# Kernel tuning notes

Hardware: AMD Instinct MI355X
Metric: run time of the kernel (lower is better)

The kernel has to match this reference:

```python
import jax, jax.numpy as jnp
import numpy as np

B = 4096
IN_DIMS = (3, 32, 32)      # in_numel = 3072
OUT_DIMS = (64, 16, 16)    # out_numel = 16384
IN_NUMEL = int(np.prod(IN_DIMS))
OUT_NUMEL = int(np.prod(OUT_DIMS))


def setup_inputs() -> dict:
    key = jax.random.key(0)
    k1, k2, k3, k4 = jax.random.split(key, 4)
    x = jax.random.normal(k1, (B,) + IN_DIMS, dtype=jnp.float32)
    # Cached composed linear operator (out_numel x in_numel); scale ~1/sqrt(fan_in)
    cached_matrix = jax.random.normal(k2, (OUT_NUMEL, IN_NUMEL), dtype=jnp.float32) / np.sqrt(IN_NUMEL)
    cached_matrix_extra = jax.random.uniform(k3, (1,), dtype=jnp.float32) + 0.5
    cached_tensor_extra = jax.random.normal(k4, (IN_NUMEL, IN_NUMEL), dtype=jnp.float32) / IN_NUMEL
    return {
        "x": x,
        "cached_matrix": cached_matrix,
        "cached_matrix_extra": cached_matrix_extra,
        "cached_tensor_extra": cached_tensor_extra,
    }


def reference(x, cached_matrix, cached_matrix_extra, cached_tensor_extra):
    batches = x.shape[0]
    # input_as_matrix: [in_numel, B]
    X = x.reshape(batches, -1).T
    # input_as_matrix_extra: L2 norm per column -> [1, B]
    X_extra = jnp.linalg.norm(X, ord=2, axis=0, keepdims=True)
    # output_as_matrix = M @ X : [out_numel, B]
    Y = jnp.matmul(cached_matrix, X)
    # output_as_matrix_extra = s * ||x|| + sum((T @ X) * X, axis=0)
    Y_extra = cached_matrix_extra * X_extra + jnp.sum(jnp.matmul(cached_tensor_extra, X) * X, axis=0, keepdims=True)
    Y = Y / Y_extra
    return Y.T.reshape(batches, *OUT_DIMS)
```

## Files before the change

kernel.cpp:

```cpp
#include <hip/hip_runtime.h>
#include <hip/hip_bf16.h>

typedef __attribute__((ext_vector_type(8))) short bf16x8;
typedef __attribute__((ext_vector_type(4))) short bf16x4;
typedef __attribute__((ext_vector_type(4))) float f32x4;

#define DEV __device__ __forceinline__

static constexpr int BATCH = 4096;
static constexpr int KDIM  = 3072;
static constexpr int NOUT  = 16384;

DEV unsigned short f2bf(float f) {
  union { float f; unsigned int u; } v; v.f = f;
  unsigned int u = v.u;
  u += 0x7fffu + ((u >> 16) & 1u);
  return (unsigned short)(u >> 16);
}

__global__ __launch_bounds__(256) void prep_x_kernel(
    const float* __restrict__ x, unsigned short* __restrict__ xbf,
    float* __restrict__ nrm) {
  const int b = blockIdx.x;
  const int t = threadIdx.x;
  const float* row = x + (size_t)b * KDIM;
  unsigned short* orow = xbf + (size_t)b * KDIM;
  float ss = 0.f;
#pragma unroll
  for (int i = 0; i < 3; ++i) {
    const int c = i * 256 + t;
    float4 v = reinterpret_cast<const float4*>(row)[c];
    ss += v.x * v.x + v.y * v.y + v.z * v.z + v.w * v.w;
    bf16x4 o;
    o[0] = (short)f2bf(v.x); o[1] = (short)f2bf(v.y);
    o[2] = (short)f2bf(v.z); o[3] = (short)f2bf(v.w);
    reinterpret_cast<bf16x4*>(orow)[c] = o;
  }
#pragma unroll
  for (int off = 32; off > 0; off >>= 1) ss += __shfl_down(ss, off, 64);
  __shared__ float red[4];
  if ((t & 63) == 0) red[t >> 6] = ss;
  __syncthreads();
  if (t == 0) nrm[b] = sqrtf(red[0] + red[1] + red[2] + red[3]);
}

__global__ __launch_bounds__(256) void cvt_kernel(
    const float* __restrict__ src, unsigned short* __restrict__ dst, size_t n4) {
  size_t i = (size_t)blockIdx.x * blockDim.x + threadIdx.x;
  const size_t stride = (size_t)gridDim.x * blockDim.x;
  for (; i < n4; i += stride) {
    float4 v = reinterpret_cast<const float4*>(src)[i];
    bf16x4 o;
    o[0] = (short)f2bf(v.x); o[1] = (short)f2bf(v.y);
    o[2] = (short)f2bf(v.z); o[3] = (short)f2bf(v.w);
    reinterpret_cast<bf16x4*>(dst)[i] = o;
  }
}

__global__ __launch_bounds__(256) void qform_kernel(
    const unsigned short* __restrict__ A,
    const unsigned short* __restrict__ Bm,
    const float* __restrict__ xf,
    float* __restrict__ partial) {
  __shared__ unsigned short ldsA[128 * 32];
  __shared__ unsigned short ldsB[128 * 32];
  const int t = threadIdx.x;
  const int lane = t & 63;
  const int wv = t >> 6;
  const int wr = wv >> 1, wc = wv & 1;
  const int col0 = blockIdx.x * 128;
  const int row0 = blockIdx.y * 128;

  f32x4 acc[4][4];
#pragma unroll
  for (int i = 0; i < 4; ++i)
#pragma unroll
    for (int j = 0; j < 4; ++j) acc[i][j] = (f32x4){0.f, 0.f, 0.f, 0.f};

  const unsigned short* aBase = A + (size_t)row0 * KDIM;
  const unsigned short* bBase = Bm + (size_t)col0 * KDIM;
  const int ldsoff0 = (t & ~63) * 8;

  for (int k0 = 0; k0 < KDIM; k0 += 32) {
    __syncthreads();
#pragma unroll
    for (int i = 0; i < 2; ++i) {
      const int c = i * 256 + t;
      const unsigned short* ga = aBase + (size_t)(c >> 2) * KDIM + (k0 + (c & 3) * 8);
      const unsigned short* gb = bBase + (size_t)(c >> 2) * KDIM + (k0 + (c & 3) * 8);
      __builtin_amdgcn_global_load_lds(
          (const __attribute__((address_space(1))) unsigned int*)(const void*)ga,
          (__attribute__((address_space(3))) unsigned int*)(void*)(ldsA + i * 2048 + ldsoff0),
          16, 0, 0);
      __builtin_amdgcn_global_load_lds(
          (const __attribute__((address_space(1))) unsigned int*)(const void*)gb,
          (__attribute__((address_space(3))) unsigned int*)(void*)(ldsB + i * 2048 + ldsoff0),
          16, 0, 0);
    }
    __syncthreads();
    bf16x8 af[4], bfr[4];
#pragma unroll
    for (int mi = 0; mi < 4; ++mi)
      af[mi] = *reinterpret_cast<const bf16x8*>(
          &ldsA[(wr * 64 + mi * 16 + (lane & 15)) * 32 + (lane >> 4) * 8]);
#pragma unroll
    for (int ni = 0; ni < 4; ++ni)
      bfr[ni] = *reinterpret_cast<const bf16x8*>(
          &ldsB[(wc * 64 + ni * 16 + (lane & 15)) * 32 + (lane >> 4) * 8]);
#pragma unroll
    for (int mi = 0; mi < 4; ++mi)
#pragma unroll
      for (int ni = 0; ni < 4; ++ni)
        acc[mi][ni] = __builtin_amdgcn_mfma_f32_16x16x32_bf16(af[mi], bfr[ni], acc[mi][ni], 0, 0, 0);
  }

#pragma unroll
  for (int mi = 0; mi < 4; ++mi) {
#pragma unroll
    for (int j = 0; j < 4; ++j) {
      const int b = row0 + wr * 64 + mi * 16 + (lane >> 4) * 4 + j;
      const float* xrow = xf + (size_t)b * KDIM + col0 + wc * 64 + (lane & 15);
      float s = 0.f;
#pragma unroll
      for (int ni = 0; ni < 4; ++ni) s += acc[mi][ni][j] * xrow[ni * 16];
      s += __shfl_xor(s, 1, 64);
      s += __shfl_xor(s, 2, 64);
      s += __shfl_xor(s, 4, 64);
      s += __shfl_xor(s, 8, 64);
      if ((lane & 15) == 0) partial[(size_t)b * 48 + blockIdx.x * 2 + wc] = s;
    }
  }
}

__global__ __launch_bounds__(256) void finalize_ye_kernel(
    const float* __restrict__ nrm, const float* __restrict__ partial,
    const float* __restrict__ sp, float* __restrict__ ye) {
  const int b = blockIdx.x * blockDim.x + threadIdx.x;
  if (b >= BATCH) return;
  float qv = 0.f;
#pragma unroll
  for (int i = 0; i < 48; ++i) qv += partial[(size_t)b * 48 + i];
  ye[b] = sp[0] * nrm[b] + qv;
}

static constexpr int BK8 = 64;
static constexpr int NKT = KDIM / BK8;

#define LDSE(BUF, OP, HALF) ((BUF)*32768 + (OP)*16384 + (HALF)*8192)

#define STAGE8(OP, HALF, S, BUF)                                             \
  {                                                                          \
    const unsigned short* gb_ = (OP) ? Bm : A;                               \
    const int gr0_ = ((OP) ? col0 : row0) + (HALF)*128;                      \
    _Pragma("unroll")                                                        \
    for (int j_ = 0; j_ < 2; ++j_) {                                         \
      const int row_ = j_*64 + wid*8 + (lane >> 3);                          \
      const int le_  = ((lane & 7)*8) ^ ((row_ & 7) << 3);                   \
      __builtin_amdgcn_global_load_lds(                                      \
        (const __attribute__((address_space(1))) unsigned int*)(const void*) \
          (gb_ + (size_t)(gr0_ + row_)*KDIM + (S)*BK8 + le_),                \
        (__attribute__((address_space(3))) unsigned int*)(void*)             \
          (lds + LDSE(BUF, OP, HALF) + j_*4096 + wid*512),                   \
        16, 0, 0);                                                           \
    }                                                                        \
  }

#define LOADFRAGS8(P, QM, QN)                                                \
  _Pragma("unroll")                                                          \
  for (int mi = 0; mi < 4; ++mi) {                                           \
    const int r_ = wm*64 + mi*16 + (lane & 15);                              \
    const int xv_ = (r_ & 7) << 3;                                           \
    _Pragma("unroll")                                                        \
    for (int ks = 0; ks < 2; ++ks)                                           \
      aft[mi][ks] = *reinterpret_cast<const bf16x8*>(                        \
          lds + LDSE(P, 0, QM) + ((r_*64 + ks*32 + (lane >> 4)*8) ^ xv_));   \
  }                                                                          \
  _Pragma("unroll")                                                          \
  for (int ni = 0; ni < 2; ++ni) {                                           \
    const int r_ = wn*32 + ni*16 + (lane & 15);                              \
    const int xv_ = (r_ & 7) << 3;                                           \
    _Pragma("unroll")                                                        \
    for (int ks = 0; ks < 2; ++ks)                                           \
      bft[ni][ks] = *reinterpret_cast<const bf16x8*>(                        \
          lds + LDSE(P, 1, QN) + ((r_*64 + ks*32 + (lane >> 4)*8) ^ xv_));   \
  }

#define MMA8(QM, QN)                                                         \
  __builtin_amdgcn_s_setprio(1);                                             \
  _Pragma("unroll")                                                          \
  for (int mi = 0; mi < 4; ++mi)                                             \
    _Pragma("unroll")                                                        \
    for (int ni = 0; ni < 2; ++ni)                                           \
      _Pragma("unroll")                                                      \
      for (int ks = 0; ks < 2; ++ks)                                         \
        acc[(QM)*4 + mi][(QN)*2 + ni] =                                      \
            __builtin_amdgcn_mfma_f32_16x16x32_bf16(                         \
                aft[mi][ks], bft[ni][ks], acc[(QM)*4 + mi][(QN)*2 + ni],     \
                0, 0, 0);                                                    \
  __builtin_amdgcn_s_setprio(0);

#define VMW(N)                                                               \
  asm volatile("s_waitcnt vmcnt(" #N ")" ::: "memory");                      \
  __builtin_amdgcn_sched_barrier(0)

#define NOVM (void)0

#define PHASE8(P, QM, QN, STAGESTMT, VMSTMT)                                 \
  LOADFRAGS8(P, QM, QN);                                                     \
  __builtin_amdgcn_s_barrier();                                              \
  STAGESTMT;                                                                 \
  MMA8(QM, QN);                                                              \
  VMSTMT;                                                                    \
  __builtin_amdgcn_s_barrier();

#define TILE8(P, T)                                                          \
  PHASE8(P, 0, 0, STAGE8(1, 1, (T) + 1, (P) ^ 1), NOVM);                     \
  PHASE8(P, 0, 1, STAGE8(0, 0, (T) + 2, P), NOVM);                           \
  PHASE8(P, 1, 0, STAGE8(1, 0, (T) + 2, P), NOVM);                           \
  PHASE8(P, 1, 1, STAGE8(0, 1, (T) + 2, P), VMW(6));

__global__ __launch_bounds__(512) void gemm8_kernel(
    const unsigned short* __restrict__ A,
    const unsigned short* __restrict__ Bm,
    const float* __restrict__ ye,
    float* __restrict__ out) {
  __shared__ unsigned short lds[65536];
  const int t = threadIdx.x;
  const int lane = t & 63, wid = t >> 6;
  const int wm = wid >> 2, wn = wid & 3;

  const int bid = blockIdx.x;
  const int wgid = (bid & 7) * 128 + (bid >> 3);
  const int bx = wgid & 63;
  const int by = wgid >> 6;
  const int row0 = by * 256, col0 = bx * 256;

  f32x4 acc[8][4];
#pragma unroll
  for (int i = 0; i < 8; ++i)
#pragma unroll
    for (int j = 0; j < 4; ++j) acc[i][j] = (f32x4){0.f, 0.f, 0.f, 0.f};

  bf16x8 aft[4][2], bft[2][2];

  STAGE8(0, 0, 0, 0); STAGE8(1, 0, 0, 0); STAGE8(0, 1, 0, 0); STAGE8(1, 1, 0, 0);
  STAGE8(0, 0, 1, 1); STAGE8(1, 0, 1, 1); STAGE8(0, 1, 1, 1);
  VMW(6);
  __builtin_amdgcn_s_barrier();

#pragma unroll 1
  for (int i = 0; i < 23; ++i) {
    const int t0 = 2 * i;
    TILE8(0, t0);
    TILE8(1, t0 + 1);
  }

  PHASE8(0, 0, 0, STAGE8(1, 1, 47, 1), NOVM);
  PHASE8(0, 0, 1, NOVM, NOVM);
  PHASE8(0, 1, 0, NOVM, NOVM);
  PHASE8(0, 1, 1, NOVM, VMW(0));
  PHASE8(1, 0, 0, NOVM, NOVM);
  PHASE8(1, 0, 1, NOVM, NOVM);
  PHASE8(1, 1, 0, NOVM, NOVM);
  PHASE8(1, 1, 1, NOVM, NOVM);

#pragma unroll
  for (int am = 0; am < 8; ++am) {
#pragma unroll
    for (int j = 0; j < 4; ++j) {
      const int b = row0 + (am >> 2) * 128 + wm * 64 + (am & 3) * 16 +
                    (lane >> 4) * 4 + j;
      const float r = 1.0f / ye[b];
      float* orow = out + (size_t)b * NOUT + col0;
#pragma unroll
      for (int an = 0; an < 4; ++an)
        orow[(an >> 1) * 128 + wn * 32 + (an & 1) * 16 + (lane & 15)] =
            acc[am][an][j] * r;
    }
  }
}

__global__ __launch_bounds__(256) void main_gemm_kernel(
    const unsigned short* __restrict__ A,
    const float* __restrict__ Bf,
    const float* __restrict__ ye,
    float* __restrict__ out) {
  __shared__ unsigned short ldsA[128 * 32];
  __shared__ unsigned short ldsB[128 * 32];
  const int t = threadIdx.x;
  const int lane = t & 63;
  const int wv = t >> 6;
  const int wr = wv >> 1, wc = wv & 1;
  const int col0 = blockIdx.x * 128;
  const int row0 = blockIdx.y * 128;

  f32x4 acc[4][4];
#pragma unroll
  for (int i = 0; i < 4; ++i)
#pragma unroll
    for (int j = 0; j < 4; ++j) acc[i][j] = (f32x4){0.f, 0.f, 0.f, 0.f};

  const unsigned short* aBase = A + (size_t)row0 * KDIM;
  const float* bfBase = Bf + (size_t)col0 * KDIM;
  const int ldsoff0 = (t & ~63) * 8;

  for (int k0 = 0; k0 < KDIM; k0 += 32) {
    __syncthreads();
#pragma unroll
    for (int i = 0; i < 2; ++i) {
      const int c = i * 256 + t;
      const unsigned short* ga = aBase + (size_t)(c >> 2) * KDIM + (k0 + (c & 3) * 8);
      __builtin_amdgcn_global_load_lds(
          (const __attribute__((address_space(1))) unsigned int*)(const void*)ga,
          (__attribute__((address_space(3))) unsigned int*)(void*)(ldsA + i * 2048 + ldsoff0),
          16, 0, 0);
    }
#pragma unroll
    for (int i = 0; i < 2; ++i) {
      const int c = i * 256 + t;
      const int r = c >> 1, ko = (c & 1) * 16;
      const float* gp = bfBase + (size_t)r * KDIM + k0 + ko;
      unsigned short tmp[16];
#pragma unroll
      for (int q = 0; q < 4; ++q) {
        float4 v = reinterpret_cast<const float4*>(gp)[q];
        tmp[q * 4 + 0] = f2bf(v.x); tmp[q * 4 + 1] = f2bf(v.y);
        tmp[q * 4 + 2] = f2bf(v.z); tmp[q * 4 + 3] = f2bf(v.w);
      }
#pragma unroll
      for (int q = 0; q < 2; ++q)
        *reinterpret_cast<bf16x8*>(&ldsB[r * 32 + ko + q * 8]) =
            *reinterpret_cast<const bf16x8*>(&tmp[q * 8]);
    }
    __syncthreads();
    bf16x8 af[4], bfr[4];
#pragma unroll
    for (int mi = 0; mi < 4; ++mi)
      af[mi] = *reinterpret_cast<const bf16x8*>(
          &ldsA[(wr * 64 + mi * 16 + (lane & 15)) * 32 + (lane >> 4) * 8]);
#pragma unroll
    for (int ni = 0; ni < 4; ++ni)
      bfr[ni] = *reinterpret_cast<const bf16x8*>(
          &ldsB[(wc * 64 + ni * 16 + (lane & 15)) * 32 + (lane >> 4) * 8]);
#pragma unroll
    for (int mi = 0; mi < 4; ++mi)
#pragma unroll
      for (int ni = 0; ni < 4; ++ni)
        acc[mi][ni] = __builtin_amdgcn_mfma_f32_16x16x32_bf16(af[mi], bfr[ni], acc[mi][ni], 0, 0, 0);
  }

#pragma unroll
  for (int mi = 0; mi < 4; ++mi) {
#pragma unroll
    for (int j = 0; j < 4; ++j) {
      const int b = row0 + wr * 64 + mi * 16 + (lane >> 4) * 4 + j;
      const float r = 1.0f / ye[b];
      float* orow = out + (size_t)b * NOUT + col0 + wc * 64 + (lane & 15);
#pragma unroll
      for (int ni = 0; ni < 4; ++ni) orow[ni * 16] = acc[mi][ni][j] * r;
    }
  }
}

extern "C" void kernel_launch(void* const* d_in, const int* in_sizes, int n_in,
                              void* d_out, int out_size, void* d_ws, size_t ws_size,
                              hipStream_t stream) {
  (void)in_sizes; (void)n_in; (void)out_size;
  const float* x  = (const float*)d_in[0];
  const float* M  = (const float*)d_in[1];
  const float* sc = (const float*)d_in[2];
  const float* T  = (const float*)d_in[3];
  float* out = (float*)d_out;
  char* ws = (char*)d_ws;

  size_t off = 0;
  auto wsalloc = [&](size_t bytes) -> void* {
    void* p = ws + off;
    off += (bytes + 255) & ~(size_t)255;
    return p;
  };
  unsigned short* Xbf = (unsigned short*)wsalloc((size_t)BATCH * KDIM * 2);
  unsigned short* Tbf = (unsigned short*)wsalloc((size_t)KDIM * KDIM * 2);
  float* nrm = (float*)wsalloc((size_t)BATCH * 4);
  float* ye  = (float*)wsalloc((size_t)BATCH * 4);
  float* partial = (float*)wsalloc((size_t)BATCH * 48 * 4);
  unsigned short* Mbf = (unsigned short*)wsalloc((size_t)NOUT * KDIM * 2);
  const bool useMbf = (off <= ws_size);

  prep_x_kernel<<<BATCH, 256, 0, stream>>>(x, Xbf, nrm);
  cvt_kernel<<<1024, 256, 0, stream>>>(T, Tbf, (size_t)KDIM * KDIM / 4);
  if (useMbf)
    cvt_kernel<<<2048, 256, 0, stream>>>(M, Mbf, (size_t)NOUT * KDIM / 4);
  qform_kernel<<<dim3(KDIM / 128, BATCH / 128), 256, 0, stream>>>(Xbf, Tbf, x, partial);
  finalize_ye_kernel<<<BATCH / 256, 256, 0, stream>>>(nrm, partial, sc, ye);
  if (useMbf)
    gemm8_kernel<<<dim3((NOUT / 256) * (BATCH / 256)), 512, 0, stream>>>(
        Xbf, Mbf, ye, out);
  else
    main_gemm_kernel<<<dim3(NOUT / 128, BATCH / 128), 256, 0, stream>>>(
        Xbf, M, ye, out);
}
```

Before: 606.9 us.

## Reorder GEMM quadrant schedule to reuse LDS fragments across MMA phases

```diff
diff --git a/kernel.cpp b/kernel.cpp
--- a/kernel.cpp
+++ b/kernel.cpp
@@ -144,7 +144,6 @@
 }
 
 static constexpr int BK8 = 64;
-static constexpr int NKT = KDIM / BK8;
 
 #define LDSE(BUF, OP, HALF) ((BUF)*32768 + (OP)*16384 + (HALF)*8192)
 
@@ -165,7 +164,7 @@
     }                                                                        \
   }
 
-#define LOADFRAGS8(P, QM, QN)                                                \
+#define LOADA8(P, QM)                                                        \
   _Pragma("unroll")                                                          \
   for (int mi = 0; mi < 4; ++mi) {                                           \
     const int r_ = wm*64 + mi*16 + (lane & 15);                              \
@@ -174,7 +173,9 @@
     for (int ks = 0; ks < 2; ++ks)                                           \
       aft[mi][ks] = *reinterpret_cast<const bf16x8*>(                        \
           lds + LDSE(P, 0, QM) + ((r_*64 + ks*32 + (lane >> 4)*8) ^ xv_));   \
-  }                                                                          \
+  }
+
+#define LOADB8(P, QN)                                                        \
   _Pragma("unroll")                                                          \
   for (int ni = 0; ni < 2; ++ni) {                                           \
     const int r_ = wn*32 + ni*16 + (lane & 15);                              \
@@ -203,21 +204,18 @@
   asm volatile("s_waitcnt vmcnt(" #N ")" ::: "memory");                      \
   __builtin_amdgcn_sched_barrier(0)
 
-#define NOVM (void)0
-
-#define PHASE8(P, QM, QN, STAGESTMT, VMSTMT)                                 \
-  LOADFRAGS8(P, QM, QN);                                                     \
-  __builtin_amdgcn_s_barrier();                                              \
-  STAGESTMT;                                                                 \
-  MMA8(QM, QN);                                                              \
-  VMSTMT;                                                                    \
-  __builtin_amdgcn_s_barrier();
+#define BARR __builtin_amdgcn_s_barrier()
 
 #define TILE8(P, T)                                                          \
-  PHASE8(P, 0, 0, STAGE8(1, 1, (T) + 1, (P) ^ 1), NOVM);                     \
-  PHASE8(P, 0, 1, STAGE8(0, 0, (T) + 2, P), NOVM);                           \
-  PHASE8(P, 1, 0, STAGE8(1, 0, (T) + 2, P), NOVM);                           \
-  PHASE8(P, 1, 1, STAGE8(0, 1, (T) + 2, P), VMW(6));
+  LOADA8(P, 0); LOADB8(P, 0);                                                \
+  STAGE8(1, 1, (T)+1, (P)^1); STAGE8(1, 0, (T)+1, (P)^1);                    \
+  BARR; MMA8(0, 0); BARR;                                                    \
+  LOADB8(P, 1); STAGE8(0, 0, (T)+2, P);                                      \
+  BARR; MMA8(0, 1); BARR;                                                    \
+  LOADA8(P, 1);                                                              \
+  BARR; MMA8(1, 1); BARR;                                                    \
+  LOADB8(P, 0); STAGE8(0, 1, (T)+2, P);                                      \
+  BARR; MMA8(1, 0); VMW(4); BARR;
 
 __global__ __launch_bounds__(512) void gemm8_kernel(
     const unsigned short* __restrict__ A,
@@ -244,9 +242,9 @@
   bf16x8 aft[4][2], bft[2][2];
 
   STAGE8(0, 0, 0, 0); STAGE8(1, 0, 0, 0); STAGE8(0, 1, 0, 0); STAGE8(1, 1, 0, 0);
-  STAGE8(0, 0, 1, 1); STAGE8(1, 0, 1, 1); STAGE8(0, 1, 1, 1);
-  VMW(6);
-  __builtin_amdgcn_s_barrier();
+  STAGE8(0, 0, 1, 1); STAGE8(0, 1, 1, 1);
+  VMW(4);
+  BARR;
 
 #pragma unroll 1
   for (int i = 0; i < 23; ++i) {
@@ -255,14 +253,23 @@
     TILE8(1, t0 + 1);
   }
 
-  PHASE8(0, 0, 0, STAGE8(1, 1, 47, 1), NOVM);
-  PHASE8(0, 0, 1, NOVM, NOVM);
-  PHASE8(0, 1, 0, NOVM, NOVM);
-  PHASE8(0, 1, 1, NOVM, VMW(0));
-  PHASE8(1, 0, 0, NOVM, NOVM);
-  PHASE8(1, 0, 1, NOVM, NOVM);
-  PHASE8(1, 1, 0, NOVM, NOVM);
-  PHASE8(1, 1, 1, NOVM, NOVM);
+  LOADA8(0, 0); LOADB8(0, 0);
+  STAGE8(1, 1, 47, 1); STAGE8(1, 0, 47, 1);
+  BARR; MMA8(0, 0); BARR;
+  LOADB8(0, 1);
+  BARR; MMA8(0, 1); BARR;
+  LOADA8(0, 1);
+  BARR; MMA8(1, 1); BARR;
+  LOADB8(0, 0);
+  BARR; MMA8(1, 0); VMW(0); BARR;
+  LOADA8(1, 0); LOADB8(1, 0);
+  BARR; MMA8(0, 0); BARR;
+  LOADB8(1, 1);
+  BARR; MMA8(0, 1); BARR;
+  LOADA8(1, 1);
+  BARR; MMA8(1, 1); BARR;
+  LOADB8(1, 0);
+  BARR; MMA8(1, 0);
 
 #pragma unroll
   for (int am = 0; am < 8; ++am) {
```

Measured after the change: 562.3 us. -7.3%, faster.
